# Performance work log

Measured on AMD Instinct MI355X. Metric: run time of the kernel, lower is better.

Reference implementation:

```python
import jax, jax.numpy as jnp
import numpy as np

NEG_SLOPE = 0.2   # PyG GATConv default negative_slope
BN_EPS = 1e-5
N_NODES = 50000
N_EDGES = 600000
N_GRAPHS = 64


def _gat_conv(x, W, att_src, att_dst, bias, src, dst, heads, out_ch, concat):
    """PyG GATConv (eval mode, self-loops already appended to src/dst).
    x: [N, in], W: [in, heads*out_ch], att_*: [heads, out_ch], bias: [heads*out_ch] or [out_ch].
    """
    n = x.shape[0]
    h = (x @ W).reshape(n, heads, out_ch)                  # [N, H, C]
    a_s = jnp.sum(h * att_src[None], axis=-1)              # [N, H]
    a_d = jnp.sum(h * att_dst[None], axis=-1)              # [N, H]
    logit = jax.nn.leaky_relu(a_s[src] + a_d[dst], NEG_SLOPE)  # [E, H]
    # segment softmax over destination node (every node has a self-loop -> no empty segment)
    m = jax.ops.segment_max(logit, dst, num_segments=n)
    p = jnp.exp(logit - m[dst])
    denom = jax.ops.segment_sum(p, dst, num_segments=n)
    alpha = p / (denom[dst] + 1e-16)                       # [E, H]
    out = jax.ops.segment_sum(h[src] * alpha[:, :, None], dst, num_segments=n)  # [N, H, C]
    out = out.reshape(n, heads * out_ch) if concat else out.mean(axis=1)
    return out + bias


def _bn(x, gamma, beta):
    mu = x.mean(axis=0)
    var = x.var(axis=0)
    return (x - mu) * jax.lax.rsqrt(var + BN_EPS) * gamma + beta


def setup_inputs() -> dict:
    key = jax.random.key(0)
    ks = jax.random.split(key, 20)
    hidden = 64
    d1_in, d1_out, h1 = 5, hidden // 2, 4          # 5 -> 32x4 = 128
    d2_in, d2_out, h2 = hidden * 2, hidden // 2, 4  # 128 -> 32x4 = 128
    d3_in, d3_out, h3 = hidden * 2, hidden, 1       # 128 -> 64

    def glorot(k, shape):
        fan = shape[0] + shape[-1]
        return jax.random.normal(k, shape, dtype=jnp.float32) * np.sqrt(2.0 / fan)

    inp = {
        "x": jax.random.normal(ks[0], (N_NODES, d1_in), dtype=jnp.float32),
        "edge_index": jax.random.randint(ks[1], (2, N_EDGES), 0, N_NODES),
        "batch": jnp.sort(jax.random.randint(ks[2], (N_NODES,), 0, N_GRAPHS)),
        # conv1
        "W1": glorot(ks[3], (d1_in, h1 * d1_out)),
        "a1_src": glorot(ks[4], (h1, d1_out)),
        "a1_dst": glorot(ks[5], (h1, d1_out)),
        "b1": jnp.zeros((h1 * d1_out,), dtype=jnp.float32),
        "g1": jnp.ones((h1 * d1_out,), dtype=jnp.float32),
        "be1": jnp.zeros((h1 * d1_out,), dtype=jnp.float32),
        # conv2
        "W2": glorot(ks[6], (d2_in, h2 * d2_out)),
        "a2_src": glorot(ks[7], (h2, d2_out)),
        "a2_dst": glorot(ks[8], (h2, d2_out)),
        "b2": jnp.zeros((h2 * d2_out,), dtype=jnp.float32),
        "g2": jnp.ones((h2 * d2_out,), dtype=jnp.float32),
        "be2": jnp.zeros((h2 * d2_out,), dtype=jnp.float32),
        # conv3 (single head, concat=False)
        "W3": glorot(ks[9], (d3_in, h3 * d3_out)),
        "a3_src": glorot(ks[10], (h3, d3_out)),
        "a3_dst": glorot(ks[11], (h3, d3_out)),
        "b3": jnp.zeros((d3_out,), dtype=jnp.float32),
    }
    return inp


def reference(x, edge_index, batch, W1, a1_src, a1_dst, b1, g1, be1,
              W2, a2_src, a2_dst, b2, g2, be2, W3, a3_src, a3_dst, b3):
    n = x.shape[0]
    loops = jnp.arange(n)
    src = jnp.concatenate([edge_index[0], loops])  # PyG add_self_loops=True
    dst = jnp.concatenate([edge_index[1], loops])

    h = jax.nn.elu(_bn(_gat_conv(x, W1, a1_src, a1_dst, b1, src, dst, 4, 32, True), g1, be1))
    h = jax.nn.elu(_bn(_gat_conv(h, W2, a2_src, a2_dst, b2, src, dst, 4, 32, True), g2, be2))
    h = jax.nn.elu(_gat_conv(h, W3, a3_src, a3_dst, b3, src, dst, 1, 64, False))

    counts = jax.ops.segment_sum(jnp.ones((n,), h.dtype), batch, num_segments=N_GRAPHS)
    mean_pool = jax.ops.segment_sum(h, batch, num_segments=N_GRAPHS) / jnp.maximum(counts, 1.0)[:, None]
    max_pool = jax.ops.segment_max(h, batch, num_segments=N_GRAPHS)
    max_pool = jnp.where(counts[:, None] > 0, max_pool, 0.0)
    return jnp.concatenate([mean_pool, max_pool], axis=1)  # [G, 128]
```

## Files before the change

kernel.cpp:

```cpp
#include <hip/hip_runtime.h>
#include <math.h>

#define NEG_SLOPE 0.2f
#define BN_EPS 1e-5f

typedef __attribute__((ext_vector_type(8))) short short8;
typedef __attribute__((ext_vector_type(4))) float f32x4;

__device__ __forceinline__ float lrelu_f(float x){ return x > 0.f ? x : NEG_SLOPE * x; }
__device__ __forceinline__ float elu_f(float x){ return x > 0.f ? x : __expf(x) - 1.f; }

__device__ __forceinline__ unsigned short f2bf(float f){
    unsigned u = __float_as_uint(f);
    return (unsigned short)((u + 0x7fffu + ((u >> 16) & 1u)) >> 16);
}
__device__ __forceinline__ float bf_lo(unsigned v){ return __uint_as_float(v << 16); }
__device__ __forceinline__ float bf_hi(unsigned v){ return __uint_as_float(v & 0xffff0000u); }
__device__ __forceinline__ float bf2f(unsigned short b){ return __uint_as_float((unsigned)b << 16); }

__device__ __forceinline__ unsigned enc_f(float x){
    unsigned b = __float_as_uint(x);
    return (b & 0x80000000u) ? ~b : (b | 0x80000000u);
}
__device__ __forceinline__ float dec_f(unsigned u){
    return __uint_as_float((u & 0x80000000u) ? (u & 0x7FFFFFFFu) : ~u);
}

__global__ void k_prep(const int* __restrict__ ei, int E0, int N, int Bc, int Bg,
                       const int* __restrict__ batch, int G,
                       int* __restrict__ counts, int* __restrict__ gp,
                       const float* __restrict__ W1, const float* __restrict__ a1s,
                       const float* __restrict__ a1d,
                       const float* __restrict__ W2, const float* __restrict__ W3,
                       unsigned short* __restrict__ wt2, unsigned short* __restrict__ wt3,
                       float* __restrict__ u_s, float* __restrict__ u_d){
    int b = blockIdx.x, tid = threadIdx.x;
    if (b < Bc){
        int i = b * 256 + tid, tot = E0 + N;
        if (i < tot){
            int dst = (i < E0) ? ei[E0 + i] : (i - E0);
            atomicAdd(&counts[dst], 1);
        }
    } else if (b < Bc + Bg){
        int i = (b - Bc) * 256 + tid;
        if (i < N){
            int bb = batch[i];
            if (i == 0){ for (int g = 0; g <= bb; ++g) gp[g] = 0; }
            else { int pb = batch[i - 1]; for (int g = pb + 1; g <= bb; ++g) gp[g] = i; }
            if (i == N - 1){ for (int g = bb + 1; g <= G; ++g) gp[g] = N; }
        }
    } else if (b < Bc + Bg + 96){
        int i = (b - Bc - Bg) * 256 + tid;
        if (i < 128 * 128){
            int k = i / 128, c = i % 128;
            wt2[c * 128 + k] = f2bf(W2[i]);
        } else if (i < 128 * 128 + 128 * 64){
            int j = i - 128 * 128;
            int k = j / 64, c = j % 64;
            wt3[c * 128 + k] = f2bf(W3[j]);
        }
    } else {
        if (tid < 40){
            int t2 = tid % 20;
            int k = t2 / 4, hh = t2 % 4;
            const float* att = (tid < 20) ? a1s : a1d;
            float s = 0.f;
            for (int j = 0; j < 32; ++j) s += W1[k * 128 + hh * 32 + j] * att[hh * 32 + j];
            if (tid < 20) u_s[k * 4 + hh] = s; else u_d[k * 4 + hh] = s;
        }
    }
}

__global__ void k_scan_part(const int* __restrict__ counts, int n, int* __restrict__ part){
    __shared__ int sh[256];
    int tid = threadIdx.x;
    int i = blockIdx.x * 256 + tid;
    int v = (i < n) ? counts[i] : 0;
    sh[tid] = v;
    __syncthreads();
    for (int o = 128; o > 0; o >>= 1){
        if (tid < o) sh[tid] += sh[tid + o];
        __syncthreads();
    }
    if (tid == 0) part[blockIdx.x] = sh[0];
}

__global__ void k_scan_write(const int* __restrict__ counts, const int* __restrict__ part,
                             int n, int* __restrict__ row_ptr){
    __shared__ int sh[256], rsh[256];
    __shared__ int offs;
    int tid = threadIdx.x, bid = blockIdx.x;
    int po = 0;
    for (int j = tid; j < bid; j += 256) po += part[j];
    rsh[tid] = po;
    __syncthreads();
    for (int o = 128; o > 0; o >>= 1){
        if (tid < o) rsh[tid] += rsh[tid + o];
        __syncthreads();
    }
    if (tid == 0) offs = rsh[0];
    __syncthreads();
    int i = bid * 256 + tid;
    int v = (i < n) ? counts[i] : 0;
    sh[tid] = v;
    __syncthreads();
    for (int o = 1; o < 256; o <<= 1){
        int t = (tid >= o) ? sh[tid - o] : 0;
        __syncthreads();
        sh[tid] += t;
        __syncthreads();
    }
    if (i < n) row_ptr[i] = offs + sh[tid] - v;
    if (bid == gridDim.x - 1 && tid == 255) row_ptr[n] = offs + sh[255];
}

__global__ void k_scatter(const int* __restrict__ ei, int E0, int N,
                          const int* __restrict__ row_ptr, int* __restrict__ cursor,
                          int* __restrict__ csr_src){
    int i = blockIdx.x * blockDim.x + threadIdx.x;
    int tot = E0 + N;
    if (i >= tot) return;
    int src, dst;
    if (i < E0){ src = ei[i]; dst = ei[E0 + i]; } else { src = dst = i - E0; }
    int pos = atomicAdd(&cursor[dst], 1);
    csr_src[row_ptr[dst] + pos] = src;
}

__launch_bounds__(256)
__global__ void k_l1(const float* __restrict__ X, const float* __restrict__ W1,
                     const float* __restrict__ u_s, const float* __restrict__ u_d,
                     const int* __restrict__ row_ptr, const int* __restrict__ csr_src,
                     const float* __restrict__ bias, unsigned short* __restrict__ out, int N){
    __shared__ float Wl[5 * 128];
    int tid = threadIdx.x;
    for (int i = tid; i < 5 * 128; i += 256) Wl[i] = W1[i];
    __syncthreads();
    int grp = tid >> 4, ln = tid & 15;
    int hh = ln >> 2, sl = ln & 3;
    long n = (long)blockIdx.x * 16 + grp;
    if (n >= N) return;
    float us[5], ud[5];
#pragma unroll
    for (int k = 0; k < 5; ++k){ us[k] = u_s[k * 4 + hh]; ud[k] = u_d[k * 4 + hh]; }
    float ad = 0.f;
#pragma unroll
    for (int k = 0; k < 5; ++k) ad += X[n * 5 + k] * ud[k];
    int beg = row_ptr[n], end = row_ptr[n + 1];
    float y0 = 0.f, y1 = 0.f, y2 = 0.f, y3 = 0.f, y4 = 0.f, dn = 0.f;
    for (int e = beg + sl; e < end; e += 4){
        long s = csr_src[e];
        float x0 = X[s * 5 + 0], x1 = X[s * 5 + 1], x2 = X[s * 5 + 2],
              x3 = X[s * 5 + 3], x4 = X[s * 5 + 4];
        float as = x0 * us[0] + x1 * us[1] + x2 * us[2] + x3 * us[3] + x4 * us[4];
        float p = __expf(lrelu_f(as + ad));
        dn += p;
        y0 += p * x0; y1 += p * x1; y2 += p * x2; y3 += p * x3; y4 += p * x4;
    }
#pragma unroll
    for (int m = 1; m < 4; m <<= 1){
        y0 += __shfl_xor(y0, m); y1 += __shfl_xor(y1, m); y2 += __shfl_xor(y2, m);
        y3 += __shfl_xor(y3, m); y4 += __shfl_xor(y4, m); dn += __shfl_xor(dn, m);
    }
    float inv = 1.f / dn;
    y0 *= inv; y1 *= inv; y2 *= inv; y3 *= inv; y4 *= inv;
    int c0 = ln * 8;
    const float4* Wl4 = (const float4*)Wl;
    float4 oa, ob;
    {
        float4 w0a = Wl4[0 * 32 + ln * 2], w0b = Wl4[0 * 32 + ln * 2 + 1];
        float4 w1a = Wl4[1 * 32 + ln * 2], w1b = Wl4[1 * 32 + ln * 2 + 1];
        float4 w2a = Wl4[2 * 32 + ln * 2], w2b = Wl4[2 * 32 + ln * 2 + 1];
        float4 w3a = Wl4[3 * 32 + ln * 2], w3b = Wl4[3 * 32 + ln * 2 + 1];
        float4 w4a = Wl4[4 * 32 + ln * 2], w4b = Wl4[4 * 32 + ln * 2 + 1];
        oa.x = y0*w0a.x + y1*w1a.x + y2*w2a.x + y3*w3a.x + y4*w4a.x + bias[c0 + 0];
        oa.y = y0*w0a.y + y1*w1a.y + y2*w2a.y + y3*w3a.y + y4*w4a.y + bias[c0 + 1];
        oa.z = y0*w0a.z + y1*w1a.z + y2*w2a.z + y3*w3a.z + y4*w4a.z + bias[c0 + 2];
        oa.w = y0*w0a.w + y1*w1a.w + y2*w2a.w + y3*w3a.w + y4*w4a.w + bias[c0 + 3];
        ob.x = y0*w0b.x + y1*w1b.x + y2*w2b.x + y3*w3b.x + y4*w4b.x + bias[c0 + 4];
        ob.y = y0*w0b.y + y1*w1b.y + y2*w2b.y + y3*w3b.y + y4*w4b.y + bias[c0 + 5];
        ob.z = y0*w0b.z + y1*w1b.z + y2*w2b.z + y3*w3b.z + y4*w4b.z + bias[c0 + 6];
        ob.w = y0*w0b.w + y1*w1b.w + y2*w2b.w + y3*w3b.w + y4*w4b.w + bias[c0 + 7];
    }
    uint4 o;
    o.x = (unsigned)f2bf(oa.x) | ((unsigned)f2bf(oa.y) << 16);
    o.y = (unsigned)f2bf(oa.z) | ((unsigned)f2bf(oa.w) << 16);
    o.z = (unsigned)f2bf(ob.x) | ((unsigned)f2bf(ob.y) << 16);
    o.w = (unsigned)f2bf(ob.z) | ((unsigned)f2bf(ob.w) << 16);
    *(uint4*)&out[n * 128 + c0] = o;
}

template<int OUT, int H, bool BN>
__launch_bounds__(256)
__global__ void k_gemm_mfma(const unsigned short* __restrict__ X, const unsigned short* __restrict__ Wt,
                            const float* __restrict__ atts, const float* __restrict__ attd,
                            const float* __restrict__ coefs, const float* __restrict__ coefb,
                            unsigned short* __restrict__ h, float* __restrict__ as_,
                            float* __restrict__ ad_, int N){
    constexpr int TM  = 64;
    constexpr int NCT = OUT / 16;
    constexpr int CPH = NCT / H;
    __shared__ unsigned short Xl[TM * 128];
    __shared__ unsigned short Wl[OUT * 128];
    int tid = threadIdx.x;
    long base = (long)blockIdx.x * TM;

    for (int i = tid; i < OUT * 16; i += 256){
        int r = i >> 4, g = i & 15;
        uint4 v = *(const uint4*)&Wt[r * 128 + g * 8];
        int gs = g ^ (r & 7);
        *(uint4*)&Wl[r * 128 + gs * 8] = v;
    }
    for (int i = tid; i < TM * 16; i += 256){
        int r = i >> 4, g = i & 15;
        long node = base + r;
        uint4 o;
        if (node < N){
            uint4 raw = *(const uint4*)&X[node * 128 + g * 8];
            float f[8];
            f[0] = bf_lo(raw.x); f[1] = bf_hi(raw.x);
            f[2] = bf_lo(raw.y); f[3] = bf_hi(raw.y);
            f[4] = bf_lo(raw.z); f[5] = bf_hi(raw.z);
            f[6] = bf_lo(raw.w); f[7] = bf_hi(raw.w);
#pragma unroll
            for (int j = 0; j < 8; ++j){
                float v = f[j];
                if (BN) v = elu_f(fmaf(v, coefs[g * 8 + j], coefb[g * 8 + j]));
                f[j] = v;
            }
            o.x = (unsigned)f2bf(f[0]) | ((unsigned)f2bf(f[1]) << 16);
            o.y = (unsigned)f2bf(f[2]) | ((unsigned)f2bf(f[3]) << 16);
            o.z = (unsigned)f2bf(f[4]) | ((unsigned)f2bf(f[5]) << 16);
            o.w = (unsigned)f2bf(f[6]) | ((unsigned)f2bf(f[7]) << 16);
        } else {
            o.x = o.y = o.z = o.w = 0u;
        }
        int gs = g ^ (r & 7);
        *(uint4*)&Xl[r * 128 + gs * 8] = o;
    }
    __syncthreads();

    int wid = tid >> 6;
    int lane = tid & 63;
    int lr = lane & 15, lk = lane >> 4;

    short8 afrag[4];
    int arow = wid * 16 + lr;
#pragma unroll
    for (int ks = 0; ks < 4; ++ks){
        int g = ks * 4 + lk;
        int gs = g ^ (arow & 7);
        afrag[ks] = *(const short8*)&Xl[arow * 128 + gs * 8];
    }
    f32x4 acc[NCT];
#pragma unroll
    for (int ct = 0; ct < NCT; ++ct) acc[ct] = (f32x4){0.f, 0.f, 0.f, 0.f};
#pragma unroll
    for (int ct = 0; ct < NCT; ++ct){
        int brow = ct * 16 + lr;
#pragma unroll
        for (int ks = 0; ks < 4; ++ks){
            int g = ks * 4 + lk;
            int gs = g ^ (brow & 7);
            short8 bfrag = *(const short8*)&Wl[brow * 128 + gs * 8];
            acc[ct] = __builtin_amdgcn_mfma_f32_16x16x32_bf16(afrag[ks], bfrag, acc[ct], 0, 0, 0);
        }
    }
    float ps[H][4], pd[H][4];
#pragma unroll
    for (int hh = 0; hh < H; ++hh)
#pragma unroll
        for (int j = 0; j < 4; ++j){ ps[hh][j] = 0.f; pd[hh][j] = 0.f; }
#pragma unroll
    for (int ct = 0; ct < NCT; ++ct){
        int col = ct * 16 + lr;
        int hh = ct / CPH;
        float asv = atts[col], adv = attd[col];
#pragma unroll
        for (int j = 0; j < 4; ++j){
            float v = acc[ct][j];
            long node = base + wid * 16 + lk * 4 + j;
            if (node < N) h[node * OUT + col] = f2bf(v);
            ps[hh][j] += v * asv;
            pd[hh][j] += v * adv;
        }
    }
#pragma unroll
    for (int m = 1; m < 16; m <<= 1){
#pragma unroll
        for (int hh = 0; hh < H; ++hh)
#pragma unroll
            for (int j = 0; j < 4; ++j){
                ps[hh][j] += __shfl_xor(ps[hh][j], m);
                pd[hh][j] += __shfl_xor(pd[hh][j], m);
            }
    }
    if (lr == 0){
#pragma unroll
        for (int j = 0; j < 4; ++j){
            long node = base + wid * 16 + lk * 4 + j;
            if (node < N){
#pragma unroll
                for (int hh = 0; hh < H; ++hh){
                    as_[node * H + hh] = ps[hh][j];
                    ad_[node * H + hh] = pd[hh][j];
                }
            }
        }
    }
}

template<int C, int H, int ACT>
__global__ void k_agg(const unsigned short* __restrict__ h, const float* __restrict__ as_,
                      const float* __restrict__ ad_, const int* __restrict__ row_ptr,
                      const int* __restrict__ csr_src, const float* __restrict__ bias,
                      unsigned short* __restrict__ out, int N){
    constexpr int CPL = C / 64;
    constexpr int GROUP = C / H;
    int n = blockIdx.x;
    if (n >= N) return;
    int lane = threadIdx.x;
    int hh = (CPL * lane) / GROUP;
    float ad = ad_[n * H + hh];
    int beg = row_ptr[n], end = row_ptr[n + 1];
    float accx = 0.f, accy = 0.f, dn = 0.f;
    const unsigned* h32 = (const unsigned*)h;
    int e = beg;
    for (; e + 2 <= end; e += 2){
        int s0 = csr_src[e], s1 = csr_src[e + 1];
        float a0 = as_[s0 * H + hh], a1 = as_[s1 * H + hh];
        unsigned v0, v1; unsigned short w0, w1;
        if (CPL == 2){ v0 = h32[(long)s0 * 64 + lane]; v1 = h32[(long)s1 * 64 + lane]; }
        else { w0 = h[(long)s0 * 64 + lane]; w1 = h[(long)s1 * 64 + lane]; }
        float p0 = __expf(lrelu_f(a0 + ad));
        float p1 = __expf(lrelu_f(a1 + ad));
        dn += p0 + p1;
        if (CPL == 2){
            accx += p0 * bf_lo(v0) + p1 * bf_lo(v1);
            accy += p0 * bf_hi(v0) + p1 * bf_hi(v1);
        } else {
            accx += p0 * bf2f(w0) + p1 * bf2f(w1);
        }
    }
    if (e < end){
        int s0 = csr_src[e];
        float p0 = __expf(lrelu_f(as_[s0 * H + hh] + ad));
        dn += p0;
        if (CPL == 2){
            unsigned v0 = h32[(long)s0 * 64 + lane];
            accx += p0 * bf_lo(v0); accy += p0 * bf_hi(v0);
        } else {
            accx += p0 * bf2f(h[(long)s0 * 64 + lane]);
        }
    }
    float inv = 1.f / dn;
    if (CPL == 2){
        float vx = accx * inv + bias[2 * lane];
        float vy = accy * inv + bias[2 * lane + 1];
        if (ACT == 1){ vx = elu_f(vx); vy = elu_f(vy); }
        ((unsigned*)out)[(long)n * 64 + lane] =
            (unsigned)f2bf(vx) | ((unsigned)f2bf(vy) << 16);
    } else {
        float v = accx * inv + bias[lane];
        if (ACT == 1) v = elu_f(v);
        out[(long)n * 64 + lane] = f2bf(v);
    }
}

__launch_bounds__(256)
__global__ void k_bn_part(const unsigned short* __restrict__ x, int N,
                          float* __restrict__ ps, float* __restrict__ pq){
    __shared__ float ls[256 * 8], lq[256 * 8];
    int tid = threadIdx.x;
    int cg = tid & 15;
    int rg = tid >> 4;
    int rpb = (N + gridDim.x - 1) / gridDim.x;
    int lo = blockIdx.x * rpb;
    int hi = lo + rpb; if (hi > N) hi = N;
    float s[8], q[8];
#pragma unroll
    for (int j = 0; j < 8; ++j){ s[j] = 0.f; q[j] = 0.f; }
    int r = lo + rg;
    for (; r + 16 < hi; r += 32){
        uint4 va = *(const uint4*)&x[(long)r * 128 + cg * 8];
        uint4 vb = *(const uint4*)&x[(long)(r + 16) * 128 + cg * 8];
        float fa[8], fb[8];
        fa[0]=bf_lo(va.x); fa[1]=bf_hi(va.x); fa[2]=bf_lo(va.y); fa[3]=bf_hi(va.y);
        fa[4]=bf_lo(va.z); fa[5]=bf_hi(va.z); fa[6]=bf_lo(va.w); fa[7]=bf_hi(va.w);
        fb[0]=bf_lo(vb.x); fb[1]=bf_hi(vb.x); fb[2]=bf_lo(vb.y); fb[3]=bf_hi(vb.y);
        fb[4]=bf_lo(vb.z); fb[5]=bf_hi(vb.z); fb[6]=bf_lo(vb.w); fb[7]=bf_hi(vb.w);
#pragma unroll
        for (int j = 0; j < 8; ++j){
            s[j] += fa[j] + fb[j];
            q[j] += fa[j] * fa[j] + fb[j] * fb[j];
        }
    }
    for (; r < hi; r += 16){
        uint4 va = *(const uint4*)&x[(long)r * 128 + cg * 8];
        float fa[8];
        fa[0]=bf_lo(va.x); fa[1]=bf_hi(va.x); fa[2]=bf_lo(va.y); fa[3]=bf_hi(va.y);
        fa[4]=bf_lo(va.z); fa[5]=bf_hi(va.z); fa[6]=bf_lo(va.w); fa[7]=bf_hi(va.w);
#pragma unroll
        for (int j = 0; j < 8; ++j){ s[j] += fa[j]; q[j] += fa[j] * fa[j]; }
    }
#pragma unroll
    for (int j = 0; j < 8; ++j){ ls[tid * 8 + j] = s[j]; lq[tid * 8 + j] = q[j]; }
    __syncthreads();
    for (int o = 8; o > 0; o >>= 1){
        if (rg < o){
#pragma unroll
            for (int j = 0; j < 8; ++j){
                s[j] += ls[(tid + o * 16) * 8 + j];
                q[j] += lq[(tid + o * 16) * 8 + j];
                ls[tid * 8 + j] = s[j]; lq[tid * 8 + j] = q[j];
            }
        }
        __syncthreads();
    }
    if (rg == 0){
#pragma unroll
        for (int j = 0; j < 8; ++j){
            ps[(long)blockIdx.x * 128 + cg * 8 + j] = s[j];
            pq[(long)blockIdx.x * 128 + cg * 8 + j] = q[j];
        }
    }
}

__launch_bounds__(1024)
__global__ void k_bn_fin(const float* __restrict__ ps, const float* __restrict__ pq, int PB,
                         const float* __restrict__ g, const float* __restrict__ be,
                         float invN, float* __restrict__ cs, float* __restrict__ cb){
    __shared__ float sh_s[1024], sh_q[1024];
    int tid = threadIdx.x;
    int c = tid & 127, sl = tid >> 7;
    float s = 0.f, q = 0.f;
    for (int b = sl; b < PB; b += 8){
        s += ps[(long)b * 128 + c];
        q += pq[(long)b * 128 + c];
    }
    sh_s[tid] = s; sh_q[tid] = q;
    __syncthreads();
    for (int o = 4; o > 0; o >>= 1){
        if (sl < o){
            s += sh_s[tid + o * 128]; q += sh_q[tid + o * 128];
            sh_s[tid] = s; sh_q[tid] = q;
        }
        __syncthreads();
    }
    if (sl == 0){
        float mu = s * invN;
        float var = q * invN - mu * mu;
        float sc = g[c] * rsqrtf(var + BN_EPS);
        cs[c] = sc;
        cb[c] = be[c] - mu * sc;
    }
}

__global__ void k_pool_part(const unsigned short* __restrict__ x, const int* __restrict__ gp,
                            float* __restrict__ psum, unsigned* __restrict__ pmax){
    constexpr int S = 16;
    __shared__ float2 ssum[256], smax[256];
    int g = blockIdx.y;
    int split = blockIdx.x;
    int tid = threadIdx.x;
    int c2 = tid & 31, sub = tid >> 5;
    int beg = gp[g], end = gp[g + 1];
    int len = end - beg;
    int chunk = (len + S - 1) / S;
    int lo = beg + split * chunk;
    int hi = lo + chunk; if (hi > end) hi = end;
    if (lo >= hi) return;
    float sx = 0.f, sy = 0.f, mx = -1e30f, my = -1e30f;
    const unsigned* xr = (const unsigned*)x;
    for (int i = lo + sub; i < hi; i += 8){
        unsigned v = xr[(long)i * 32 + c2];
        float a = bf_lo(v), b = bf_hi(v);
        sx += a; sy += b;
        mx = fmaxf(mx, a); my = fmaxf(my, b);
    }
    ssum[tid] = make_float2(sx, sy); smax[tid] = make_float2(mx, my);
    __syncthreads();
    for (int o = 4; o > 0; o >>= 1){
        if (sub < o){
            float2 s2 = ssum[tid + o * 32], m2 = smax[tid + o * 32];
            sx += s2.x; sy += s2.y;
            mx = fmaxf(mx, m2.x); my = fmaxf(my, m2.y);
            ssum[tid] = make_float2(sx, sy); smax[tid] = make_float2(mx, my);
        }
        __syncthreads();
    }
    if (sub == 0){
        atomicAdd(&psum[g * 64 + c2 * 2], sx);
        atomicAdd(&psum[g * 64 + c2 * 2 + 1], sy);
        atomicMax(&pmax[g * 64 + c2 * 2], enc_f(mx));
        atomicMax(&pmax[g * 64 + c2 * 2 + 1], enc_f(my));
    }
}

__global__ void k_pool_fin(const float* __restrict__ psum, const unsigned* __restrict__ pmax,
                           const int* __restrict__ gp, float* __restrict__ out){
    int g = blockIdx.x;
    int c = threadIdx.x;
    int cnt = gp[g + 1] - gp[g];
    float mean = (cnt > 0) ? psum[g * 64 + c] / (float)cnt : 0.f;
    float mx   = (cnt > 0) ? dec_f(pmax[g * 64 + c]) : 0.f;
    out[g * 128 + c]      = mean;
    out[g * 128 + 64 + c] = mx;
}

extern "C" void kernel_launch(void* const* d_in, const int* in_sizes, int n_in,
                              void* d_out, int out_size, void* d_ws, size_t ws_size,
                              hipStream_t stream){
    const float* x   = (const float*)d_in[0];
    const int*   ei  = (const int*)d_in[1];
    const int*   bat = (const int*)d_in[2];
    const float* W1  = (const float*)d_in[3];
    const float* a1s = (const float*)d_in[4];
    const float* a1d = (const float*)d_in[5];
    const float* b1  = (const float*)d_in[6];
    const float* g1  = (const float*)d_in[7];
    const float* be1 = (const float*)d_in[8];
    const float* W2  = (const float*)d_in[9];
    const float* a2s = (const float*)d_in[10];
    const float* a2d = (const float*)d_in[11];
    const float* b2  = (const float*)d_in[12];
    const float* g2  = (const float*)d_in[13];
    const float* be2 = (const float*)d_in[14];
    const float* W3  = (const float*)d_in[15];
    const float* a3s = (const float*)d_in[16];
    const float* a3d = (const float*)d_in[17];
    const float* b3  = (const float*)d_in[18];
    float* out = (float*)d_out;

    int N  = in_sizes[2];
    int E0 = in_sizes[1] / 2;
    int E  = E0 + N;
    const int G = 64;
    int P  = (N + 255) / 256;
    const int PB = 512;

    char* ws = (char*)d_ws;
    size_t off = 0;
    auto alloc = [&](size_t bytes) -> char* {
        char* p = ws + off;
        off += (bytes + 255) & ~(size_t)255;
        return p;
    };
    int*      counts  = (int*)alloc((size_t)N * 4);
    int*      cursor  = (int*)alloc((size_t)N * 4);
    float*    psum    = (float*)alloc((size_t)G * 64 * 4);
    unsigned* pmax    = (unsigned*)alloc((size_t)G * 64 * 4);
    size_t zero_bytes = off;
    int*   part    = (int*)alloc(256 * 4);
    int*   row_ptr = (int*)alloc((size_t)(N + 1) * 4);
    int*   csr     = (int*)alloc((size_t)E * 4);
    int*   gp      = (int*)alloc((size_t)(G + 1) * 4);
    float* as_buf  = (float*)alloc((size_t)N * 4 * 4);
    float* ad_buf  = (float*)alloc((size_t)N * 4 * 4);
    float* coefs   = (float*)alloc(128 * 4);
    float* coefb   = (float*)alloc(128 * 4);
    float* u_s     = (float*)alloc(20 * 4);
    float* u_d     = (float*)alloc(20 * 4);
    float* bn_ps   = (float*)alloc((size_t)PB * 128 * 4);
    float* bn_pq   = (float*)alloc((size_t)PB * 128 * 4);
    unsigned short* wt2 = (unsigned short*)alloc(128 * 128 * 2);
    unsigned short* wt3 = (unsigned short*)alloc(64 * 128 * 2);
    unsigned short* hbuf = (unsigned short*)alloc((size_t)N * 128 * 2);
    unsigned short* xcur = (unsigned short*)alloc((size_t)N * 128 * 2);

    hipMemsetAsync(ws, 0, zero_bytes, stream);

    int Bc = (E + 255) / 256, Bg = (N + 255) / 256;
    k_prep<<<Bc + Bg + 96 + 1, 256, 0, stream>>>(ei, E0, N, Bc, Bg, bat, G, counts, gp,
                                                 W1, a1s, a1d, W2, W3, wt2, wt3, u_s, u_d);
    k_scan_part<<<P, 256, 0, stream>>>(counts, N, part);
    k_scan_write<<<P, 256, 0, stream>>>(counts, part, N, row_ptr);
    k_scatter<<<(E + 255) / 256, 256, 0, stream>>>(ei, E0, N, row_ptr, cursor, csr);

    k_l1<<<(N + 15) / 16, 256, 0, stream>>>(x, W1, u_s, u_d, row_ptr, csr, b1, xcur, N);
    k_bn_part<<<PB, 256, 0, stream>>>(xcur, N, bn_ps, bn_pq);
    k_bn_fin<<<1, 1024, 0, stream>>>(bn_ps, bn_pq, PB, g1, be1, 1.f / N, coefs, coefb);

    k_gemm_mfma<128, 4, true><<<(N + 63) / 64, 256, 0, stream>>>(
        xcur, wt2, a2s, a2d, coefs, coefb, hbuf, as_buf, ad_buf, N);
    k_agg<128, 4, 0><<<N, 64, 0, stream>>>(hbuf, as_buf, ad_buf, row_ptr, csr, b2, xcur, N);
    k_bn_part<<<PB, 256, 0, stream>>>(xcur, N, bn_ps, bn_pq);
    k_bn_fin<<<1, 1024, 0, stream>>>(bn_ps, bn_pq, PB, g2, be2, 1.f / N, coefs, coefb);

    k_gemm_mfma<64, 1, true><<<(N + 63) / 64, 256, 0, stream>>>(
        xcur, wt3, a3s, a3d, coefs, coefb, hbuf, as_buf, ad_buf, N);
    k_agg<64, 1, 1><<<N, 64, 0, stream>>>(hbuf, as_buf, ad_buf, row_ptr, csr, b3, xcur, N);

    {
        dim3 grid(16, G);
        k_pool_part<<<grid, 256, 0, stream>>>(xcur, gp, psum, pmax);
        k_pool_fin<<<G, 64, 0, stream>>>(psum, pmax, gp, out);
    }
}
```

Measured before the change: 233.1 us.

## Fuse layer-1 BN stats into aggregation, merge scan, use exp2 and unrolled agg

```diff
diff --git a/kernel.cpp b/kernel.cpp
--- a/kernel.cpp
+++ b/kernel.cpp
@@ -3,6 +3,7 @@
 
 #define NEG_SLOPE 0.2f
 #define BN_EPS 1e-5f
+#define LOG2E 1.44269504088896f
 
 typedef __attribute__((ext_vector_type(8))) short short8;
 typedef __attribute__((ext_vector_type(4))) float f32x4;
@@ -66,32 +67,19 @@
             const float* att = (tid < 20) ? a1s : a1d;
             float s = 0.f;
             for (int j = 0; j < 32; ++j) s += W1[k * 128 + hh * 32 + j] * att[hh * 32 + j];
+            s *= LOG2E;
             if (tid < 20) u_s[k * 4 + hh] = s; else u_d[k * 4 + hh] = s;
         }
     }
 }
 
-__global__ void k_scan_part(const int* __restrict__ counts, int n, int* __restrict__ part){
-    __shared__ int sh[256];
-    int tid = threadIdx.x;
-    int i = blockIdx.x * 256 + tid;
-    int v = (i < n) ? counts[i] : 0;
-    sh[tid] = v;
-    __syncthreads();
-    for (int o = 128; o > 0; o >>= 1){
-        if (tid < o) sh[tid] += sh[tid + o];
-        __syncthreads();
-    }
-    if (tid == 0) part[blockIdx.x] = sh[0];
-}
-
-__global__ void k_scan_write(const int* __restrict__ counts, const int* __restrict__ part,
-                             int n, int* __restrict__ row_ptr){
+__global__ void k_scan(const int* __restrict__ counts, int n, int* __restrict__ row_ptr){
     __shared__ int sh[256], rsh[256];
     __shared__ int offs;
     int tid = threadIdx.x, bid = blockIdx.x;
+    int limit = bid * 256;
     int po = 0;
-    for (int j = tid; j < bid; j += 256) po += part[j];
+    for (int j = tid; j < limit; j += 256) po += counts[j];
     rsh[tid] = po;
     __syncthreads();
     for (int o = 128; o > 0; o >>= 1){
@@ -100,7 +88,7 @@
     }
     if (tid == 0) offs = rsh[0];
     __syncthreads();
-    int i = bid * 256 + tid;
+    int i = limit + tid;
     int v = (i < n) ? counts[i] : 0;
     sh[tid] = v;
     __syncthreads();
@@ -130,29 +118,34 @@
 __global__ void k_l1(const float* __restrict__ X, const float* __restrict__ W1,
                      const float* __restrict__ u_s, const float* __restrict__ u_d,
                      const int* __restrict__ row_ptr, const int* __restrict__ csr_src,
-                     const float* __restrict__ bias, unsigned short* __restrict__ out, int N){
+                     const float* __restrict__ bias, unsigned short* __restrict__ out,
+                     float* __restrict__ bnb_s, float* __restrict__ bnb_q, int N){
     __shared__ float Wl[5 * 128];
+    __shared__ float bs[16][128], bq[16][128];
     int tid = threadIdx.x;
     for (int i = tid; i < 5 * 128; i += 256) Wl[i] = W1[i];
     __syncthreads();
     int grp = tid >> 4, ln = tid & 15;
     int hh = ln >> 2, sl = ln & 3;
     long n = (long)blockIdx.x * 16 + grp;
-    if (n >= N) return;
+    bool valid = n < N;
     float us[5], ud[5];
 #pragma unroll
     for (int k = 0; k < 5; ++k){ us[k] = u_s[k * 4 + hh]; ud[k] = u_d[k * 4 + hh]; }
     float ad = 0.f;
-#pragma unroll
-    for (int k = 0; k < 5; ++k) ad += X[n * 5 + k] * ud[k];
-    int beg = row_ptr[n], end = row_ptr[n + 1];
+    if (valid){
+#pragma unroll
+        for (int k = 0; k < 5; ++k) ad += X[n * 5 + k] * ud[k];
+    }
+    int beg = 0, end = 0;
+    if (valid){ beg = row_ptr[n]; end = row_ptr[n + 1]; }
     float y0 = 0.f, y1 = 0.f, y2 = 0.f, y3 = 0.f, y4 = 0.f, dn = 0.f;
     for (int e = beg + sl; e < end; e += 4){
         long s = csr_src[e];
         float x0 = X[s * 5 + 0], x1 = X[s * 5 + 1], x2 = X[s * 5 + 2],
               x3 = X[s * 5 + 3], x4 = X[s * 5 + 4];
         float as = x0 * us[0] + x1 * us[1] + x2 * us[2] + x3 * us[3] + x4 * us[4];
-        float p = __expf(lrelu_f(as + ad));
+        float p = exp2f(lrelu_f(as + ad));
         dn += p;
         y0 += p * x0; y1 += p * x1; y2 += p * x2; y3 += p * x3; y4 += p * x4;
     }
@@ -161,12 +154,12 @@
         y0 += __shfl_xor(y0, m); y1 += __shfl_xor(y1, m); y2 += __shfl_xor(y2, m);
         y3 += __shfl_xor(y3, m); y4 += __shfl_xor(y4, m); dn += __shfl_xor(dn, m);
     }
-    float inv = 1.f / dn;
+    float inv = valid ? 1.f / dn : 0.f;
     y0 *= inv; y1 *= inv; y2 *= inv; y3 *= inv; y4 *= inv;
     int c0 = ln * 8;
     const float4* Wl4 = (const float4*)Wl;
-    float4 oa, ob;
-    {
+    float4 oa = {0,0,0,0}, ob = {0,0,0,0};
+    if (valid){
         float4 w0a = Wl4[0 * 32 + ln * 2], w0b = Wl4[0 * 32 + ln * 2 + 1];
         float4 w1a = Wl4[1 * 32 + ln * 2], w1b = Wl4[1 * 32 + ln * 2 + 1];
         float4 w2a = Wl4[2 * 32 + ln * 2], w2b = Wl4[2 * 32 + ln * 2 + 1];
@@ -178,15 +171,38 @@
         oa.w = y0*w0a.w + y1*w1a.w + y2*w2a.w + y3*w3a.w + y4*w4a.w + bias[c0 + 3];
         ob.x = y0*w0b.x + y1*w1b.x + y2*w2b.x + y3*w3b.x + y4*w4b.x + bias[c0 + 4];
         ob.y = y0*w0b.y + y1*w1b.y + y2*w2b.y + y3*w3b.y + y4*w4b.y + bias[c0 + 5];
+        ob.z = y0*w0b.z + y1*w1b.z + y2*w2b.z + y3*w3b.z + y4*w2b.z*0.f + y4*w4b.z + bias[c0 + 6] - y4*w4b.z;
+        ob.w = y0*w0b.w + y1*w1b.w + y2*w2b.w + y3*w3b.w + y4*w4b.w + bias[c0 + 7];
         ob.z = y0*w0b.z + y1*w1b.z + y2*w2b.z + y3*w3b.z + y4*w4b.z + bias[c0 + 6];
-        ob.w = y0*w0b.w + y1*w1b.w + y2*w2b.w + y3*w3b.w + y4*w4b.w + bias[c0 + 7];
-    }
-    uint4 o;
-    o.x = (unsigned)f2bf(oa.x) | ((unsigned)f2bf(oa.y) << 16);
-    o.y = (unsigned)f2bf(oa.z) | ((unsigned)f2bf(oa.w) << 16);
-    o.z = (unsigned)f2bf(ob.x) | ((unsigned)f2bf(ob.y) << 16);
-    o.w = (unsigned)f2bf(ob.z) | ((unsigned)f2bf(ob.w) << 16);
-    *(uint4*)&out[n * 128 + c0] = o;
+        uint4 o;
+        o.x = (unsigned)f2bf(oa.x) | ((unsigned)f2bf(oa.y) << 16);
+        o.y = (unsigned)f2bf(oa.z) | ((unsigned)f2bf(oa.w) << 16);
+        o.z = (unsigned)f2bf(ob.x) | ((unsigned)f2bf(ob.y) << 16);
+        o.w = (unsigned)f2bf(ob.z) | ((unsigned)f2bf(ob.w) << 16);
+        *(uint4*)&out[n * 128 + c0] = o;
+    }
+    float ov[8] = {oa.x, oa.y, oa.z, oa.w, ob.x, ob.y, ob.z, ob.w};
+#pragma unroll
+    for (int j = 0; j < 8; ++j){ bs[grp][c0 + j] = ov[j]; bq[grp][c0 + j] = ov[j] * ov[j]; }
+    __syncthreads();
+    for (int o = 8; o > 0; o >>= 1){
+        if (grp < o){
+#pragma unroll
+            for (int j = 0; j < 8; ++j){
+                bs[grp][c0 + j] += bs[grp + o][c0 + j];
+                bq[grp][c0 + j] += bq[grp + o][c0 + j];
+            }
+        }
+        __syncthreads();
+    }
+    if (grp == 0){
+        int bucket = blockIdx.x & 255;
+#pragma unroll
+        for (int j = 0; j < 8; ++j){
+            atomicAdd(&bnb_s[bucket * 128 + c0 + j], bs[0][c0 + j]);
+            atomicAdd(&bnb_q[bucket * 128 + c0 + j], bq[0][c0 + j]);
+        }
+    }
 }
 
 template<int OUT, int H, bool BN>
@@ -274,7 +290,7 @@
     for (int ct = 0; ct < NCT; ++ct){
         int col = ct * 16 + lr;
         int hh = ct / CPH;
-        float asv = atts[col], adv = attd[col];
+        float asv = atts[col] * LOG2E, adv = attd[col] * LOG2E;
 #pragma unroll
         for (int j = 0; j < 4; ++j){
             float v = acc[ct][j];
@@ -309,61 +325,88 @@
     }
 }
 
-template<int C, int H, int ACT>
-__global__ void k_agg(const unsigned short* __restrict__ h, const float* __restrict__ as_,
-                      const float* __restrict__ ad_, const int* __restrict__ row_ptr,
-                      const int* __restrict__ csr_src, const float* __restrict__ bias,
-                      unsigned short* __restrict__ out, int N){
-    constexpr int CPL = C / 64;
-    constexpr int GROUP = C / H;
+__launch_bounds__(64)
+__global__ void k_agg2(const unsigned short* __restrict__ h, const float* __restrict__ as_,
+                       const float* __restrict__ ad_, const int* __restrict__ row_ptr,
+                       const int* __restrict__ csr_src, const float* __restrict__ bias,
+                       unsigned short* __restrict__ out, int N){
     int n = blockIdx.x;
     if (n >= N) return;
     int lane = threadIdx.x;
-    int hh = (CPL * lane) / GROUP;
-    float ad = ad_[n * H + hh];
+    int hh = lane >> 4;
+    float ad = ad_[n * 4 + hh];
     int beg = row_ptr[n], end = row_ptr[n + 1];
     float accx = 0.f, accy = 0.f, dn = 0.f;
     const unsigned* h32 = (const unsigned*)h;
     int e = beg;
-    for (; e + 2 <= end; e += 2){
-        int s0 = csr_src[e], s1 = csr_src[e + 1];
-        float a0 = as_[s0 * H + hh], a1 = as_[s1 * H + hh];
-        unsigned v0, v1; unsigned short w0, w1;
-        if (CPL == 2){ v0 = h32[(long)s0 * 64 + lane]; v1 = h32[(long)s1 * 64 + lane]; }
-        else { w0 = h[(long)s0 * 64 + lane]; w1 = h[(long)s1 * 64 + lane]; }
-        float p0 = __expf(lrelu_f(a0 + ad));
-        float p1 = __expf(lrelu_f(a1 + ad));
-        dn += p0 + p1;
-        if (CPL == 2){
-            accx += p0 * bf_lo(v0) + p1 * bf_lo(v1);
-            accy += p0 * bf_hi(v0) + p1 * bf_hi(v1);
-        } else {
-            accx += p0 * bf2f(w0) + p1 * bf2f(w1);
-        }
-    }
-    if (e < end){
+    for (; e < end && (e & 3); ++e){
         int s0 = csr_src[e];
-        float p0 = __expf(lrelu_f(as_[s0 * H + hh] + ad));
-        dn += p0;
-        if (CPL == 2){
-            unsigned v0 = h32[(long)s0 * 64 + lane];
-            accx += p0 * bf_lo(v0); accy += p0 * bf_hi(v0);
-        } else {
-            accx += p0 * bf2f(h[(long)s0 * 64 + lane]);
-        }
+        unsigned v0 = h32[(long)s0 * 64 + lane];
+        float p0 = exp2f(lrelu_f(as_[s0 * 4 + hh] + ad));
+        dn += p0; accx += p0 * bf_lo(v0); accy += p0 * bf_hi(v0);
+    }
+    for (; e + 4 <= end; e += 4){
+        int4 s4 = *(const int4*)&csr_src[e];
+        float a0 = as_[s4.x * 4 + hh], a1 = as_[s4.y * 4 + hh],
+              a2 = as_[s4.z * 4 + hh], a3 = as_[s4.w * 4 + hh];
+        unsigned v0 = h32[(long)s4.x * 64 + lane], v1 = h32[(long)s4.y * 64 + lane],
+                 v2 = h32[(long)s4.z * 64 + lane], v3 = h32[(long)s4.w * 64 + lane];
+        float p0 = exp2f(lrelu_f(a0 + ad));
+        float p1 = exp2f(lrelu_f(a1 + ad));
+        float p2 = exp2f(lrelu_f(a2 + ad));
+        float p3 = exp2f(lrelu_f(a3 + ad));
+        dn += p0 + p1 + p2 + p3;
+        accx += p0*bf_lo(v0) + p1*bf_lo(v1) + p2*bf_lo(v2) + p3*bf_lo(v3);
+        accy += p0*bf_hi(v0) + p1*bf_hi(v1) + p2*bf_hi(v2) + p3*bf_hi(v3);
+    }
+    for (; e < end; ++e){
+        int s0 = csr_src[e];
+        unsigned v0 = h32[(long)s0 * 64 + lane];
+        float p0 = exp2f(lrelu_f(as_[s0 * 4 + hh] + ad));
+        dn += p0; accx += p0 * bf_lo(v0); accy += p0 * bf_hi(v0);
     }
     float inv = 1.f / dn;
-    if (CPL == 2){
-        float vx = accx * inv + bias[2 * lane];
-        float vy = accy * inv + bias[2 * lane + 1];
-        if (ACT == 1){ vx = elu_f(vx); vy = elu_f(vy); }
-        ((unsigned*)out)[(long)n * 64 + lane] =
-            (unsigned)f2bf(vx) | ((unsigned)f2bf(vy) << 16);
-    } else {
-        float v = accx * inv + bias[lane];
-        if (ACT == 1) v = elu_f(v);
-        out[(long)n * 64 + lane] = f2bf(v);
-    }
+    float vx = accx * inv + bias[2 * lane];
+    float vy = accy * inv + bias[2 * lane + 1];
+    ((unsigned*)out)[(long)n * 64 + lane] = (unsigned)f2bf(vx) | ((unsigned)f2bf(vy) << 16);
+}
+
+__launch_bounds__(64)
+__global__ void k_agg3(const unsigned short* __restrict__ h, const float* __restrict__ as_,
+                       const float* __restrict__ ad_, const int* __restrict__ row_ptr,
+                       const int* __restrict__ csr_src, const float* __restrict__ bias,
+                       unsigned short* __restrict__ out, int N){
+    int n = blockIdx.x;
+    if (n >= N) return;
+    int lane = threadIdx.x;
+    float ad = ad_[n];
+    int beg = row_ptr[n], end = row_ptr[n + 1];
+    float acc = 0.f, dn = 0.f;
+    int e = beg;
+    for (; e < end && (e & 3); ++e){
+        int s0 = csr_src[e];
+        float p0 = exp2f(lrelu_f(as_[s0] + ad));
+        dn += p0; acc += p0 * bf2f(h[(long)s0 * 64 + lane]);
+    }
+    for (; e + 4 <= end; e += 4){
+        int4 s4 = *(const int4*)&csr_src[e];
+        float a0 = as_[s4.x], a1 = as_[s4.y], a2 = as_[s4.z], a3 = as_[s4.w];
+        unsigned short w0 = h[(long)s4.x * 64 + lane], w1 = h[(long)s4.y * 64 + lane],
+                       w2 = h[(long)s4.z * 64 + lane], w3 = h[(long)s4.w * 64 + lane];
+        float p0 = exp2f(lrelu_f(a0 + ad));
+        float p1 = exp2f(lrelu_f(a1 + ad));
+        float p2 = exp2f(lrelu_f(a2 + ad));
+        float p3 = exp2f(lrelu_f(a3 + ad));
+        dn += p0 + p1 + p2 + p3;
+        acc += p0*bf2f(w0) + p1*bf2f(w1) + p2*bf2f(w2) + p3*bf2f(w3);
+    }
+    for (; e < end; ++e){
+        int s0 = csr_src[e];
+        float p0 = exp2f(lrelu_f(as_[s0] + ad));
+        dn += p0; acc += p0 * bf2f(h[(long)s0 * 64 + lane]);
+    }
+    float v = elu_f(acc / dn + bias[lane]);
+    out[(long)n * 64 + lane] = f2bf(v);
 }
 
 __launch_bounds__(256)
@@ -425,23 +468,24 @@
     }
 }
 
-__launch_bounds__(1024)
+__launch_bounds__(256)
 __global__ void k_bn_fin(const float* __restrict__ ps, const float* __restrict__ pq, int PB,
                          const float* __restrict__ g, const float* __restrict__ be,
                          float invN, float* __restrict__ cs, float* __restrict__ cb){
-    __shared__ float sh_s[1024], sh_q[1024];
+    __shared__ float sh_s[256], sh_q[256];
     int tid = threadIdx.x;
-    int c = tid & 127, sl = tid >> 7;
+    int cl = tid & 15, sl = tid >> 4;
+    int c = blockIdx.x * 16 + cl;
     float s = 0.f, q = 0.f;
-    for (int b = sl; b < PB; b += 8){
+    for (int b = sl; b < PB; b += 16){
         s += ps[(long)b * 128 + c];
         q += pq[(long)b * 128 + c];
     }
     sh_s[tid] = s; sh_q[tid] = q;
     __syncthreads();
-    for (int o = 4; o > 0; o >>= 1){
+    for (int o = 8; o > 0; o >>= 1){
         if (sl < o){
-            s += sh_s[tid + o * 128]; q += sh_q[tid + o * 128];
+            s += sh_s[tid + o * 16]; q += sh_q[tid + o * 16];
             sh_s[tid] = s; sh_q[tid] = q;
         }
         __syncthreads();
@@ -536,7 +580,8 @@
     int E  = E0 + N;
     const int G = 64;
     int P  = (N + 255) / 256;
-    const int PB = 512;
+    const int NB = 256;
+    const int PB2 = 512;
 
     char* ws = (char*)d_ws;
     size_t off = 0;
@@ -549,8 +594,9 @@
     int*      cursor  = (int*)alloc((size_t)N * 4);
     float*    psum    = (float*)alloc((size_t)G * 64 * 4);
     unsigned* pmax    = (unsigned*)alloc((size_t)G * 64 * 4);
+    float*    bnb1_s  = (float*)alloc((size_t)NB * 128 * 4);
+    float*    bnb1_q  = (float*)alloc((size_t)NB * 128 * 4);
     size_t zero_bytes = off;
-    int*   part    = (int*)alloc(256 * 4);
     int*   row_ptr = (int*)alloc((size_t)(N + 1) * 4);
     int*   csr     = (int*)alloc((size_t)E * 4);
     int*   gp      = (int*)alloc((size_t)(G + 1) * 4);
@@ -560,8 +606,8 @@
     float* coefb   = (float*)alloc(128 * 4);
     float* u_s     = (float*)alloc(20 * 4);
     float* u_d     = (float*)alloc(20 * 4);
-    float* bn_ps   = (float*)alloc((size_t)PB * 128 * 4);
-    float* bn_pq   = (float*)alloc((size_t)PB * 128 * 4);
+    float* bn_ps   = (float*)alloc((size_t)PB2 * 128 * 4);
+    float* bn_pq   = (float*)alloc((size_t)PB2 * 128 * 4);
     unsigned short* wt2 = (unsigned short*)alloc(128 * 128 * 2);
     unsigned short* wt3 = (unsigned short*)alloc(64 * 128 * 2);
     unsigned short* hbuf = (unsigned short*)alloc((size_t)N * 128 * 2);
@@ -572,24 +618,22 @@
     int Bc = (E + 255) / 256, Bg = (N + 255) / 256;
     k_prep<<<Bc + Bg + 96 + 1, 256, 0, stream>>>(ei, E0, N, Bc, Bg, bat, G, counts, gp,
                                                  W1, a1s, a1d, W2, W3, wt2, wt3, u_s, u_d);
-    k_scan_part<<<P, 256, 0, stream>>>(counts, N, part);
-    k_scan_write<<<P, 256, 0, stream>>>(counts, part, N, row_ptr);
+    k_scan<<<P, 256, 0, stream>>>(counts, N, row_ptr);
     k_scatter<<<(E + 255) / 256, 256, 0, stream>>>(ei, E0, N, row_ptr, cursor, csr);
 
-    k_l1<<<(N + 15) / 16, 256, 0, stream>>>(x, W1, u_s, u_d, row_ptr, csr, b1, xcur, N);
-    k_bn_part<<<PB, 256, 0, stream>>>(xcur, N, bn_ps, bn_pq);
-    k_bn_fin<<<1, 1024, 0, stream>>>(bn_ps, bn_pq, PB, g1, be1, 1.f / N, coefs, coefb);
+    k_l1<<<(N + 15) / 16, 256, 0, stream>>>(x, W1, u_s, u_d, row_ptr, csr, b1, xcur,
+                                            bnb1_s, bnb1_q, N);
+    k_bn_fin<<<8, 256, 0, stream>>>(bnb1_s, bnb1_q, NB, g1, be1, 1.f / N, coefs, coefb);
 
     k_gemm_mfma<128, 4, true><<<(N + 63) / 64, 256, 0, stream>>>(
         xcur, wt2, a2s, a2d, coefs, coefb, hbuf, as_buf, ad_buf, N);
-    k_agg<128, 4, 0><<<N, 64, 0, stream>>>(hbuf, as_buf, ad_buf, row_ptr, csr, b2, xcur, N);
-    k_bn_part<<<PB, 256, 0, stream>>>(xcur, N, bn_ps, bn_pq);
-    k_bn_fin<<<1, 1024, 0, stream>>>(bn_ps, bn_pq, PB, g2, be2, 1.f / N, coefs, coefb);
+    k_agg2<<<N, 64, 0, stream>>>(hbuf, as_buf, ad_buf, row_ptr, csr, b2, xcur, N);
+    k_bn_part<<<PB2, 256, 0, stream>>>(xcur, N, bn_ps, bn_pq);
+    k_bn_fin<<<8, 256, 0, stream>>>(bn_ps, bn_pq, PB2, g2, be2, 1.f / N, coefs, coefb);
 
     k_gemm_mfma<64, 1, true><<<(N + 63) / 64, 256, 0, stream>>>(
         xcur, wt3, a3s, a3d, coefs, coefb, hbuf, as_buf, ad_buf, N);
-    k_agg<64, 1, 1><<<N, 64, 0, stream>>>(hbuf, as_buf, ad_buf, row_ptr, csr, b3, xcur, N);
-
+    k_agg3<<<N, 64, 0, stream>>>(hbuf, as_buf, ad_buf, row_ptr, csr, b3, xcur, N);
     {
         dim3 grid(16, G);
         k_pool_part<<<grid, 256, 0, stream>>>(xcur, gp, psum, pmax);
```

Measured after the change: 254.8 us. +9.3%, slower.

## Merge scan kernels, fold log2e into attention, parallelize BN finalize

Applied to the files above, without the earlier changes.

```diff
diff --git a/kernel.cpp b/kernel.cpp
--- a/kernel.cpp
+++ b/kernel.cpp
@@ -3,6 +3,7 @@
 
 #define NEG_SLOPE 0.2f
 #define BN_EPS 1e-5f
+#define LOG2E 1.44269504088896f
 
 typedef __attribute__((ext_vector_type(8))) short short8;
 typedef __attribute__((ext_vector_type(4))) float f32x4;
@@ -66,32 +67,19 @@
             const float* att = (tid < 20) ? a1s : a1d;
             float s = 0.f;
             for (int j = 0; j < 32; ++j) s += W1[k * 128 + hh * 32 + j] * att[hh * 32 + j];
+            s *= LOG2E;
             if (tid < 20) u_s[k * 4 + hh] = s; else u_d[k * 4 + hh] = s;
         }
     }
 }
 
-__global__ void k_scan_part(const int* __restrict__ counts, int n, int* __restrict__ part){
-    __shared__ int sh[256];
-    int tid = threadIdx.x;
-    int i = blockIdx.x * 256 + tid;
-    int v = (i < n) ? counts[i] : 0;
-    sh[tid] = v;
-    __syncthreads();
-    for (int o = 128; o > 0; o >>= 1){
-        if (tid < o) sh[tid] += sh[tid + o];
-        __syncthreads();
-    }
-    if (tid == 0) part[blockIdx.x] = sh[0];
-}
-
-__global__ void k_scan_write(const int* __restrict__ counts, const int* __restrict__ part,
-                             int n, int* __restrict__ row_ptr){
+__global__ void k_scan(const int* __restrict__ counts, int n, int* __restrict__ row_ptr){
     __shared__ int sh[256], rsh[256];
     __shared__ int offs;
     int tid = threadIdx.x, bid = blockIdx.x;
+    int limit = bid * 256;
     int po = 0;
-    for (int j = tid; j < bid; j += 256) po += part[j];
+    for (int j = tid; j < limit; j += 256) po += counts[j];
     rsh[tid] = po;
     __syncthreads();
     for (int o = 128; o > 0; o >>= 1){
@@ -100,7 +88,7 @@
     }
     if (tid == 0) offs = rsh[0];
     __syncthreads();
-    int i = bid * 256 + tid;
+    int i = limit + tid;
     int v = (i < n) ? counts[i] : 0;
     sh[tid] = v;
     __syncthreads();
@@ -152,7 +140,7 @@
         float x0 = X[s * 5 + 0], x1 = X[s * 5 + 1], x2 = X[s * 5 + 2],
               x3 = X[s * 5 + 3], x4 = X[s * 5 + 4];
         float as = x0 * us[0] + x1 * us[1] + x2 * us[2] + x3 * us[3] + x4 * us[4];
-        float p = __expf(lrelu_f(as + ad));
+        float p = exp2f(lrelu_f(as + ad));
         dn += p;
         y0 += p * x0; y1 += p * x1; y2 += p * x2; y3 += p * x3; y4 += p * x4;
     }
@@ -165,22 +153,20 @@
     y0 *= inv; y1 *= inv; y2 *= inv; y3 *= inv; y4 *= inv;
     int c0 = ln * 8;
     const float4* Wl4 = (const float4*)Wl;
+    float4 w0a = Wl4[0 * 32 + ln * 2], w0b = Wl4[0 * 32 + ln * 2 + 1];
+    float4 w1a = Wl4[1 * 32 + ln * 2], w1b = Wl4[1 * 32 + ln * 2 + 1];
+    float4 w2a = Wl4[2 * 32 + ln * 2], w2b = Wl4[2 * 32 + ln * 2 + 1];
+    float4 w3a = Wl4[3 * 32 + ln * 2], w3b = Wl4[3 * 32 + ln * 2 + 1];
+    float4 w4a = Wl4[4 * 32 + ln * 2], w4b = Wl4[4 * 32 + ln * 2 + 1];
     float4 oa, ob;
-    {
-        float4 w0a = Wl4[0 * 32 + ln * 2], w0b = Wl4[0 * 32 + ln * 2 + 1];
-        float4 w1a = Wl4[1 * 32 + ln * 2], w1b = Wl4[1 * 32 + ln * 2 + 1];
-        float4 w2a = Wl4[2 * 32 + ln * 2], w2b = Wl4[2 * 32 + ln * 2 + 1];
-        float4 w3a = Wl4[3 * 32 + ln * 2], w3b = Wl4[3 * 32 + ln * 2 + 1];
-        float4 w4a = Wl4[4 * 32 + ln * 2], w4b = Wl4[4 * 32 + ln * 2 + 1];
-        oa.x = y0*w0a.x + y1*w1a.x + y2*w2a.x + y3*w3a.x + y4*w4a.x + bias[c0 + 0];
-        oa.y = y0*w0a.y + y1*w1a.y + y2*w2a.y + y3*w3a.y + y4*w4a.y + bias[c0 + 1];
-        oa.z = y0*w0a.z + y1*w1a.z + y2*w2a.z + y3*w3a.z + y4*w4a.z + bias[c0 + 2];
-        oa.w = y0*w0a.w + y1*w1a.w + y2*w2a.w + y3*w3a.w + y4*w4a.w + bias[c0 + 3];
-        ob.x = y0*w0b.x + y1*w1b.x + y2*w2b.x + y3*w3b.x + y4*w4b.x + bias[c0 + 4];
-        ob.y = y0*w0b.y + y1*w1b.y + y2*w2b.y + y3*w3b.y + y4*w4b.y + bias[c0 + 5];
-        ob.z = y0*w0b.z + y1*w1b.z + y2*w2b.z + y3*w3b.z + y4*w4b.z + bias[c0 + 6];
-        ob.w = y0*w0b.w + y1*w1b.w + y2*w2b.w + y3*w3b.w + y4*w4b.w + bias[c0 + 7];
-    }
+    oa.x = y0*w0a.x + y1*w1a.x + y2*w2a.x + y3*w3a.x + y4*w4a.x + bias[c0 + 0];
+    oa.y = y0*w0a.y + y1*w1a.y + y2*w2a.y + y3*w3a.y + y4*w4a.y + bias[c0 + 1];
+    oa.z = y0*w0a.z + y1*w1a.z + y2*w2a.z + y3*w3a.z + y4*w4a.z + bias[c0 + 2];
+    oa.w = y0*w0a.w + y1*w1a.w + y2*w2a.w + y3*w3a.w + y4*w4a.w + bias[c0 + 3];
+    ob.x = y0*w0b.x + y1*w1b.x + y2*w2b.x + y3*w3b.x + y4*w4b.x + bias[c0 + 4];
+    ob.y = y0*w0b.y + y1*w1b.y + y2*w2b.y + y3*w3b.y + y4*w4b.y + bias[c0 + 5];
+    ob.z = y0*w0b.z + y1*w1b.z + y2*w2b.z + y3*w3b.z + y4*w4b.z + bias[c0 + 6];
+    ob.w = y0*w0b.w + y1*w1b.w + y2*w2b.w + y3*w3b.w + y4*w4b.w + bias[c0 + 7];
     uint4 o;
     o.x = (unsigned)f2bf(oa.x) | ((unsigned)f2bf(oa.y) << 16);
     o.y = (unsigned)f2bf(oa.z) | ((unsigned)f2bf(oa.w) << 16);
@@ -274,7 +260,7 @@
     for (int ct = 0; ct < NCT; ++ct){
         int col = ct * 16 + lr;
         int hh = ct / CPH;
-        float asv = atts[col], adv = attd[col];
+        float asv = atts[col] * LOG2E, adv = attd[col] * LOG2E;
 #pragma unroll
         for (int j = 0; j < 4; ++j){
             float v = acc[ct][j];
@@ -310,6 +296,7 @@
 }
 
 template<int C, int H, int ACT>
+__launch_bounds__(64)
 __global__ void k_agg(const unsigned short* __restrict__ h, const float* __restrict__ as_,
                       const float* __restrict__ ad_, const int* __restrict__ row_ptr,
                       const int* __restrict__ csr_src, const float* __restrict__ bias,
@@ -331,8 +318,8 @@
         unsigned v0, v1; unsigned short w0, w1;
         if (CPL == 2){ v0 = h32[(long)s0 * 64 + lane]; v1 = h32[(long)s1 * 64 + lane]; }
         else { w0 = h[(long)s0 * 64 + lane]; w1 = h[(long)s1 * 64 + lane]; }
-        float p0 = __expf(lrelu_f(a0 + ad));
-        float p1 = __expf(lrelu_f(a1 + ad));
+        float p0 = exp2f(lrelu_f(a0 + ad));
+        float p1 = exp2f(lrelu_f(a1 + ad));
         dn += p0 + p1;
         if (CPL == 2){
             accx += p0 * bf_lo(v0) + p1 * bf_lo(v1);
@@ -343,7 +330,7 @@
     }
     if (e < end){
         int s0 = csr_src[e];
-        float p0 = __expf(lrelu_f(as_[s0 * H + hh] + ad));
+        float p0 = exp2f(lrelu_f(as_[s0 * H + hh] + ad));
         dn += p0;
         if (CPL == 2){
             unsigned v0 = h32[(long)s0 * 64 + lane];
@@ -425,23 +412,24 @@
     }
 }
 
-__launch_bounds__(1024)
+__launch_bounds__(256)
 __global__ void k_bn_fin(const float* __restrict__ ps, const float* __restrict__ pq, int PB,
                          const float* __restrict__ g, const float* __restrict__ be,
                          float invN, float* __restrict__ cs, float* __restrict__ cb){
-    __shared__ float sh_s[1024], sh_q[1024];
+    __shared__ float sh_s[256], sh_q[256];
     int tid = threadIdx.x;
-    int c = tid & 127, sl = tid >> 7;
+    int cl = tid & 15, sl = tid >> 4;
+    int c = blockIdx.x * 16 + cl;
     float s = 0.f, q = 0.f;
-    for (int b = sl; b < PB; b += 8){
+    for (int b = sl; b < PB; b += 16){
         s += ps[(long)b * 128 + c];
         q += pq[(long)b * 128 + c];
     }
     sh_s[tid] = s; sh_q[tid] = q;
     __syncthreads();
-    for (int o = 4; o > 0; o >>= 1){
+    for (int o = 8; o > 0; o >>= 1){
         if (sl < o){
-            s += sh_s[tid + o * 128]; q += sh_q[tid + o * 128];
+            s += sh_s[tid + o * 16]; q += sh_q[tid + o * 16];
             sh_s[tid] = s; sh_q[tid] = q;
         }
         __syncthreads();
@@ -550,7 +538,6 @@
     float*    psum    = (float*)alloc((size_t)G * 64 * 4);
     unsigned* pmax    = (unsigned*)alloc((size_t)G * 64 * 4);
     size_t zero_bytes = off;
-    int*   part    = (int*)alloc(256 * 4);
     int*   row_ptr = (int*)alloc((size_t)(N + 1) * 4);
     int*   csr     = (int*)alloc((size_t)E * 4);
     int*   gp      = (int*)alloc((size_t)(G + 1) * 4);
@@ -572,24 +559,22 @@
     int Bc = (E + 255) / 256, Bg = (N + 255) / 256;
     k_prep<<<Bc + Bg + 96 + 1, 256, 0, stream>>>(ei, E0, N, Bc, Bg, bat, G, counts, gp,
                                                  W1, a1s, a1d, W2, W3, wt2, wt3, u_s, u_d);
-    k_scan_part<<<P, 256, 0, stream>>>(counts, N, part);
-    k_scan_write<<<P, 256, 0, stream>>>(counts, part, N, row_ptr);
+    k_scan<<<P, 256, 0, stream>>>(counts, N, row_ptr);
     k_scatter<<<(E + 255) / 256, 256, 0, stream>>>(ei, E0, N, row_ptr, cursor, csr);
 
     k_l1<<<(N + 15) / 16, 256, 0, stream>>>(x, W1, u_s, u_d, row_ptr, csr, b1, xcur, N);
     k_bn_part<<<PB, 256, 0, stream>>>(xcur, N, bn_ps, bn_pq);
-    k_bn_fin<<<1, 1024, 0, stream>>>(bn_ps, bn_pq, PB, g1, be1, 1.f / N, coefs, coefb);
+    k_bn_fin<<<8, 256, 0, stream>>>(bn_ps, bn_pq, PB, g1, be1, 1.f / N, coefs, coefb);
 
     k_gemm_mfma<128, 4, true><<<(N + 63) / 64, 256, 0, stream>>>(
         xcur, wt2, a2s, a2d, coefs, coefb, hbuf, as_buf, ad_buf, N);
     k_agg<128, 4, 0><<<N, 64, 0, stream>>>(hbuf, as_buf, ad_buf, row_ptr, csr, b2, xcur, N);
     k_bn_part<<<PB, 256, 0, stream>>>(xcur, N, bn_ps, bn_pq);
-    k_bn_fin<<<1, 1024, 0, stream>>>(bn_ps, bn_pq, PB, g2, be2, 1.f / N, coefs, coefb);
+    k_bn_fin<<<8, 256, 0, stream>>>(bn_ps, bn_pq, PB, g2, be2, 1.f / N, coefs, coefb);
 
     k_gemm_mfma<64, 1, true><<<(N + 63) / 64, 256, 0, stream>>>(
         xcur, wt3, a3s, a3d, coefs, coefb, hbuf, as_buf, ad_buf, N);
     k_agg<64, 1, 1><<<N, 64, 0, stream>>>(hbuf, as_buf, ad_buf, row_ptr, csr, b3, xcur, N);
-
     {
         dim3 grid(16, G);
         k_pool_part<<<grid, 256, 0, stream>>>(xcur, gp, psum, pmax);
```

After: 243.5 us (median of 2 runs). +4.5%, slower.
